# Optimization experiments

Hardware: AMD Instinct MI355X
Metric: run time of the kernel (lower is better)

## Reference

```python
import jax, jax.numpy as jnp
import numpy as np


def setup_inputs() -> dict:
    key = jax.random.key(0)
    k0, k1, k2, k3 = jax.random.split(key, 4)
    B, in_dim, n_vars, out_dim, E = 64, 512, 512, 720, 8
    x = jax.random.normal(k0, (B, in_dim, n_vars), dtype=jnp.float32)
    # Gating: nn.Linear(in_dim, E, bias=False) -> weight [E, in_dim]
    Wg = jax.random.normal(k1, (E, in_dim), dtype=jnp.float32) * 0.02
    # Experts: nn.Linear(in_dim, out_dim) -> weight [out_dim, in_dim], bias [out_dim]
    We = jax.random.normal(k2, (E, out_dim, in_dim), dtype=jnp.float32) * 0.02
    be = jax.random.normal(k3, (E, out_dim), dtype=jnp.float32) * 0.02
    return {"x": x, "Wg": Wg, "We": We, "be": be, "top_k": 2}


def reference(x, Wg, We, be, top_k):
    # x: [B, in_len, n_vars] -> tokens along n_vars with feature dim in_len
    xt = jnp.swapaxes(x, 1, 2)                      # [B, V, D]
    gate = jax.nn.softmax(xt @ Wg.T, axis=-1)       # [B, V, E]
    weights, sel = jax.lax.top_k(gate, top_k)       # [B, V, k]
    E, O, D = We.shape
    out = jnp.zeros(xt.shape[:2] + (O,), dtype=xt.dtype)  # [B, V, O]
    for e in range(E):
        # combine weight for expert e: sum over top-k slots routed to e
        coef = jnp.sum(jnp.where(sel == e, weights, jnp.zeros_like(weights)), axis=-1)  # [B, V]
        out = out + coef[..., None] * (jnp.einsum('bvd,od->bvo', xt, We[e]) + be[e])
    return jnp.swapaxes(out, 1, 2)                  # [B, pred_len, n_vars]
```

## Files before the change

### kernel.cpp

```cpp
#include <hip/hip_runtime.h>
#include <hip/hip_bf16.h>

#define DID 512
#define NV  512
#define NB  64
#define OD  720
#define OPAD 768
#define NE  8
#define NTOK (NB * NV)
#define MAXTILE 512

typedef short  bf16x8 __attribute__((ext_vector_type(8)));
typedef float  f32x4  __attribute__((ext_vector_type(4)));

#define XT_OFF    0u
#define WB_OFF    33554432u
#define PID_OFF   39845888u
#define C1D_OFF   39976960u
#define C2D_OFF   40108032u
#define TL_OFF    40239104u
#define CL1_OFF   40370176u
#define CL2_OFF   40501248u
#define BCNT_OFF  40632320u
#define BFILL_OFF 40632576u
#define BOFF_OFF  40632832u
#define TPID_OFF  40633088u
#define TT0_OFF   40635136u
#define TEND_OFF  40637184u
#define NT_OFF    40639232u
#define SCR_OFF   40639488u
#define SCR_END   87825408u

static __device__ __forceinline__ ushort f2bf(float f) {
  unsigned u = __float_as_uint(f);
  unsigned r = (u + 0x7fffu + ((u >> 16) & 1u)) >> 16;
  return (ushort)r;
}
static __device__ __forceinline__ float bf2f(ushort u) {
  return __uint_as_float(((unsigned)u) << 16);
}
static __device__ __forceinline__ void async16(const ushort* g, ushort* l) {
  __builtin_amdgcn_global_load_lds((__attribute__((address_space(1))) void*)(g),
                                   (__attribute__((address_space(3))) void*)(l),
                                   16, 0, 0);
}
static __device__ __forceinline__ int swz(int r) { return (r & 3) ^ ((r >> 2) & 1); }

__global__ __launch_bounds__(256) void k_transpose(const float* __restrict__ x,
                                                   ushort* __restrict__ xt) {
  __shared__ float s[32][33];
  const int b  = blockIdx.z;
  const int v0 = blockIdx.x * 32;
  const int d0 = blockIdx.y * 32;
  const int tx = threadIdx.x & 31;
  const int ty = threadIdx.x >> 5;
  const float* xp = x + ((size_t)b * DID + d0 + ty) * NV + v0 + tx;
#pragma unroll
  for (int i = 0; i < 4; ++i) s[ty + i * 8][tx] = xp[(size_t)i * 8 * NV];
  __syncthreads();
#pragma unroll
  for (int i = 0; i < 4; ++i) {
    int vl = ty + i * 8;
    xt[((size_t)b * NV + v0 + vl) * DID + d0 + tx] = f2bf(s[tx][vl]);
  }
}

__global__ __launch_bounds__(256) void k_wbconv(const float* __restrict__ We,
                                                ushort* __restrict__ wb) {
  const int e = blockIdx.y;
  const int i = blockIdx.x * 256 + threadIdx.x;
  const int o = i >> 9;
  ushort val = 0;
  if (o < OD) val = f2bf(We[(size_t)e * OD * DID + i]);
  wb[(size_t)e * OPAD * DID + i] = val;
}

__global__ __launch_bounds__(256) void k_gate(const float* __restrict__ x,
                                              const float* __restrict__ Wg,
                                              int* __restrict__ pairid,
                                              float* __restrict__ c1d,
                                              float* __restrict__ c2d,
                                              int* __restrict__ bcnt) {
  __shared__ float wg[NE * DID];
  __shared__ int cnt64[64];
  const int tid = threadIdx.x;
  for (int i = tid; i < NE * DID; i += 256) wg[i] = Wg[i];
  if (tid < 64) cnt64[tid] = 0;
  __syncthreads();

  const int b = blockIdx.y;
  const int v = blockIdx.x * 256 + tid;
  const float* xp = x + (size_t)b * DID * NV + v;

  float acc[NE];
#pragma unroll
  for (int e = 0; e < NE; ++e) acc[e] = 0.f;
  for (int d = 0; d < DID; d += 4) {
    float x0 = xp[(size_t)(d + 0) * NV];
    float x1 = xp[(size_t)(d + 1) * NV];
    float x2 = xp[(size_t)(d + 2) * NV];
    float x3 = xp[(size_t)(d + 3) * NV];
#pragma unroll
    for (int e = 0; e < NE; ++e) {
      float4 w4 = *(const float4*)&wg[e * DID + d];
      acc[e] += x0 * w4.x + x1 * w4.y + x2 * w4.z + x3 * w4.w;
    }
  }
  float mx = acc[0];
#pragma unroll
  for (int e = 1; e < NE; ++e) mx = fmaxf(mx, acc[e]);
  float sum = 0.f;
#pragma unroll
  for (int e = 0; e < NE; ++e) { acc[e] = __expf(acc[e] - mx); sum += acc[e]; }
  const float inv = 1.f / sum;

  int i1 = 0; float g1 = acc[0];
#pragma unroll
  for (int e = 1; e < NE; ++e) if (acc[e] > g1) { g1 = acc[e]; i1 = e; }
  int i2 = -1; float g2 = -1.f;
#pragma unroll
  for (int e = 0; e < NE; ++e) if (e != i1 && acc[e] > g2) { g2 = acc[e]; i2 = e; }
  g1 *= inv; g2 *= inv;

  int ea, eb; float ca, cb;
  if (i1 < i2) { ea = i1; eb = i2; ca = g1; cb = g2; }
  else         { ea = i2; eb = i1; ca = g2; cb = g1; }
  const int pid = ea * 8 + eb;
  const int t = b * NV + v;
  pairid[t] = pid; c1d[t] = ca; c2d[t] = cb;
  atomicAdd(&cnt64[pid], 1);
  __syncthreads();
  if (tid < 64 && cnt64[tid]) atomicAdd(&bcnt[tid], cnt64[tid]);
}

__global__ void k_prefix(const int* __restrict__ bcnt, int* __restrict__ boffs,
                         int* __restrict__ tpid, int* __restrict__ tt0,
                         int* __restrict__ tend, int* __restrict__ ntp) {
  if (threadIdx.x != 0) return;
  int off = 0, nt = 0;
  for (int p = 0; p < 64; ++p) {
    boffs[p] = off;
    const int c = bcnt[p];
    const int end = off + c;
    for (int i = 0; i * 128 < c; ++i) {
      tpid[nt] = p; tt0[nt] = off + i * 128; tend[nt] = end; ++nt;
    }
    off = end;
  }
  ntp[0] = nt;
}

__global__ __launch_bounds__(256) void k_scatter(const int* __restrict__ pairid,
                                                 const float* __restrict__ c1d,
                                                 const float* __restrict__ c2d,
                                                 const int* __restrict__ boffs,
                                                 int* __restrict__ bfill,
                                                 int* __restrict__ tlist,
                                                 float* __restrict__ cl1,
                                                 float* __restrict__ cl2) {
  __shared__ int cnt64[64], base64[64];
  const int tid = threadIdx.x;
  if (tid < 64) cnt64[tid] = 0;
  __syncthreads();
  const int t = blockIdx.x * 256 + tid;
  const int pid = pairid[t];
  const int p = atomicAdd(&cnt64[pid], 1);
  __syncthreads();
  if (tid < 64) base64[tid] = cnt64[tid] ? atomicAdd(&bfill[tid], cnt64[tid]) : 0;
  __syncthreads();
  const int slot = boffs[pid] + base64[pid] + p;
  tlist[slot] = t; cl1[slot] = c1d[t]; cl2[slot] = c2d[t];
}

__global__ __launch_bounds__(256, 2) void k_gemm(
    const ushort* __restrict__ xt, const ushort* __restrict__ wb,
    const float* __restrict__ be, const int* __restrict__ tlist,
    const float* __restrict__ cl1, const float* __restrict__ cl2,
    const int* __restrict__ tpid, const int* __restrict__ tt0,
    const int* __restrict__ tendarr, const int* __restrict__ ntp,
    ushort* __restrict__ scratch, float* __restrict__ out, int mode) {
  const int tile = blockIdx.x;
  if (tile >= ntp[0]) return;
  const int pid  = tpid[tile];
  const int t0   = tt0[tile];
  const int tend = tendarr[tile];
  const int e1 = pid >> 3, e2 = pid & 7;
  const int o0 = blockIdx.y * 128;

  __shared__ __align__(16) ushort As[2][4096];
  __shared__ __align__(16) ushort Bs[2][4096];

  const int tid  = threadIdx.x;
  const int lane = tid & 63;
  const int w    = tid >> 6;

  const int f0 = w * 128 + lane, f1 = f0 + 64;
  const int r0 = f0 >> 2, p0 = f0 & 3, q0 = p0 ^ swz(r0);
  const int r1 = f1 >> 2, p1 = f1 & 3, q1 = p1 ^ swz(r1);

  const int aoff0 = (o0 + r0) * DID + q0 * 8;
  const int aoff1 = (o0 + r1) * DID + q1 * 8;
  const int sl0 = t0 + r0, sl1 = t0 + r1;
  const int tok0 = (sl0 < tend) ? tlist[sl0] : 0;
  const int tok1 = (sl1 < tend) ? tlist[sl1] : 0;
  const int boff0 = tok0 * DID + q0 * 8;
  const int boff1 = tok1 * DID + q1 * 8;
  const int dA0 = w * 1024, dA1 = w * 1024 + 512;

  const int m    = lane & 15;
  const int quad = lane >> 4;
  const int wo   = (w >> 1) * 64;
  const int wt   = (w & 1) * 64;

  f32x4 acc[4][4];
#pragma unroll
  for (int i = 0; i < 4; ++i)
#pragma unroll
    for (int j = 0; j < 4; ++j) acc[i][j] = (f32x4){0.f, 0.f, 0.f, 0.f};

  {
    const ushort* wA = wb + (size_t)e1 * OPAD * DID;
    async16(wA + aoff0, &As[0][dA0]);
    async16(wA + aoff1, &As[0][dA1]);
    async16(xt + boff0, &Bs[0][dA0]);
    async16(xt + boff1, &Bs[0][dA1]);
  }

  for (int kk = 0; kk < 32; ++kk) {
    __syncthreads();

    if (kk == 16) {
      float ratio[4];
#pragma unroll
      for (int j = 0; j < 4; ++j) {
        const int sl = t0 + wt + j * 16 + m;
        const bool g = sl < tend;
        const float cc1 = g ? cl1[sl] : 0.f;
        const float cc2 = g ? cl2[sl] : 1.f;
        ratio[j] = cc1 / cc2;
      }
      const float* be1p = be + e1 * OD;
#pragma unroll
      for (int i = 0; i < 4; ++i) {
        const int ob = o0 + wo + i * 16 + quad * 4;
        float b0 = 0, b1 = 0, b2 = 0, b3 = 0;
        if (ob < OD) { b0 = be1p[ob]; b1 = be1p[ob + 1]; b2 = be1p[ob + 2]; b3 = be1p[ob + 3]; }
#pragma unroll
        for (int j = 0; j < 4; ++j) {
          acc[i][j][0] = (acc[i][j][0] + b0) * ratio[j];
          acc[i][j][1] = (acc[i][j][1] + b1) * ratio[j];
          acc[i][j][2] = (acc[i][j][2] + b2) * ratio[j];
          acc[i][j][3] = (acc[i][j][3] + b3) * ratio[j];
        }
      }
    }

    const int nk = kk + 1;
    if (nk < 32) {
      const int nb = nk & 1;
      const int eA = (nk < 16) ? e1 : e2;
      const int k0 = (nk & 15) * 32;
      const ushort* wA = wb + (size_t)eA * OPAD * DID + k0;
      async16(wA + aoff0, &As[nb][dA0]);
      async16(wA + aoff1, &As[nb][dA1]);
      async16(xt + boff0 + k0, &Bs[nb][dA0]);
      async16(xt + boff1 + k0, &Bs[nb][dA1]);
    }

    const int cb = kk & 1;
    bf16x8 af[4], bfr[4];
#pragma unroll
    for (int i = 0; i < 4; ++i) {
      const int R = wo + i * 16 + m;
      af[i] = *(const bf16x8*)(&As[cb][R * 32 + ((quad ^ swz(R)) << 3)]);
    }
#pragma unroll
    for (int j = 0; j < 4; ++j) {
      const int R = wt + j * 16 + m;
      bfr[j] = *(const bf16x8*)(&Bs[cb][R * 32 + ((quad ^ swz(R)) << 3)]);
    }
#pragma unroll
    for (int i = 0; i < 4; ++i)
#pragma unroll
      for (int j = 0; j < 4; ++j)
        acc[i][j] = __builtin_amdgcn_mfma_f32_16x16x32_bf16(af[i], bfr[j],
                                                            acc[i][j], 0, 0, 0);
  }

  float c2v[4]; int tokv[4]; bool gv[4];
#pragma unroll
  for (int j = 0; j < 4; ++j) {
    const int sl = t0 + wt + j * 16 + m;
    gv[j] = sl < tend;
    c2v[j]  = gv[j] ? cl2[sl] : 0.f;
    tokv[j] = gv[j] ? tlist[sl] : 0;
  }
  const float* be2p = be + e2 * OD;
#pragma unroll
  for (int i = 0; i < 4; ++i) {
    const int ob = o0 + wo + i * 16 + quad * 4;
    if (ob < OD) {
      const float b0 = be2p[ob], b1 = be2p[ob + 1], b2 = be2p[ob + 2], b3 = be2p[ob + 3];
#pragma unroll
      for (int j = 0; j < 4; ++j) {
        if (gv[j]) {
          const float v0 = c2v[j] * (acc[i][j][0] + b0);
          const float v1 = c2v[j] * (acc[i][j][1] + b1);
          const float v2 = c2v[j] * (acc[i][j][2] + b2);
          const float v3 = c2v[j] * (acc[i][j][3] + b3);
          if (mode == 0) {
            ushort4 pk = make_ushort4(f2bf(v0), f2bf(v1), f2bf(v2), f2bf(v3));
            *(ushort4*)(scratch + (size_t)tokv[j] * OD + ob) = pk;
          } else {
            const int bb = tokv[j] >> 9, vv = tokv[j] & 511;
            float* op = out + ((size_t)bb * OD + ob) * NV + vv;
            op[0] = v0; op[(size_t)NV] = v1; op[2 * (size_t)NV] = v2; op[3 * (size_t)NV] = v3;
          }
        }
      }
    }
  }
}

__global__ __launch_bounds__(256) void k_combine(const ushort* __restrict__ scratch,
                                                 float* __restrict__ out) {
  __shared__ ushort s[64][68];
  const int v0 = blockIdx.x * 64;
  const int o0 = blockIdx.y * 64;
  const int b  = blockIdx.z;
  const int tid = threadIdx.x;
#pragma unroll
  for (int it = 0; it < 2; ++it) {
    const int c = it * 256 + tid;
    const int row = c >> 3, cg = c & 7;
    const int o = o0 + cg * 8;
    if (o + 8 <= OD) {
      const ushort* src = scratch + ((size_t)(b * NV + v0 + row)) * OD + o;
      ushort4 ua = *(const ushort4*)(src);
      ushort4 ub = *(const ushort4*)(src + 4);
      *(ushort4*)&s[row][cg * 8] = ua;
      *(ushort4*)&s[row][cg * 8 + 4] = ub;
    }
  }
  __syncthreads();
  const int vv = tid & 63;
  const int og = tid >> 6;
#pragma unroll
  for (int oi = 0; oi < 8; ++oi) {
    const int ol = (og * 8 + oi) * 2;
    const int o = o0 + ol;
    if (o < OD) {
      ushort2 u = *(const ushort2*)&s[vv][ol];
      float* op = out + ((size_t)b * OD + o) * NV + v0 + vv;
      op[0]  = bf2f(u.x);
      op[NV] = bf2f(u.y);
    }
  }
}

extern "C" void kernel_launch(void* const* d_in, const int* in_sizes, int n_in,
                              void* d_out, int out_size, void* d_ws, size_t ws_size,
                              hipStream_t stream) {
  const float* x  = (const float*)d_in[0];
  const float* Wg = (const float*)d_in[1];
  const float* We = (const float*)d_in[2];
  const float* be = (const float*)d_in[3];
  float* out = (float*)d_out;

  char* ws = (char*)d_ws;
  ushort* xt     = (ushort*)(ws + XT_OFF);
  ushort* wb     = (ushort*)(ws + WB_OFF);
  int*    pairid = (int*)   (ws + PID_OFF);
  float*  c1d    = (float*) (ws + C1D_OFF);
  float*  c2d    = (float*) (ws + C2D_OFF);
  int*    tlist  = (int*)   (ws + TL_OFF);
  float*  cl1    = (float*) (ws + CL1_OFF);
  float*  cl2    = (float*) (ws + CL2_OFF);
  int*    bcnt   = (int*)   (ws + BCNT_OFF);
  int*    bfill  = (int*)   (ws + BFILL_OFF);
  int*    boffs  = (int*)   (ws + BOFF_OFF);
  int*    tpid   = (int*)   (ws + TPID_OFF);
  int*    tt0    = (int*)   (ws + TT0_OFF);
  int*    tend   = (int*)   (ws + TEND_OFF);
  int*    ntp    = (int*)   (ws + NT_OFF);
  ushort* scratch= (ushort*)(ws + SCR_OFF);

  const int mode = (ws_size >= (size_t)SCR_END) ? 0 : 1;

  (void)hipMemsetAsync(bcnt, 0, 512, stream);

  k_transpose<<<dim3(NV / 32, DID / 32, NB), 256, 0, stream>>>(x, xt);
  k_wbconv<<<dim3(OPAD * DID / 256, NE), 256, 0, stream>>>(We, wb);
  k_gate<<<dim3(NV / 256, NB), 256, 0, stream>>>(x, Wg, pairid, c1d, c2d, bcnt);
  k_prefix<<<1, 64, 0, stream>>>(bcnt, boffs, tpid, tt0, tend, ntp);
  k_scatter<<<NTOK / 256, 256, 0, stream>>>(pairid, c1d, c2d, boffs, bfill,
                                            tlist, cl1, cl2);
  k_gemm<<<dim3(320, OPAD / 128), 256, 0, stream>>>(xt, wb, be, tlist, cl1, cl2,
                                                    tpid, tt0, tend, ntp,
                                                    scratch, out, mode);
  if (mode == 0)
    k_combine<<<dim3(NV / 64, (OD + 63) / 64, NB), 256, 0, stream>>>(scratch, out);
}
```

Before: 340.2 us.

## Fuse prep kernels, parallelize prefix scan, reorder GEMM grid, unswizzled LDS layout

Merges the transpose, weight conversion and counter memset into one k_prep launch. It also replaces the serial single-thread prefix with a wave-level shuffle scan, and swaps the GEMM grid axes so consecutive blocks share a token tile across output tiles. The GEMM LDS staging now uses a fragment-ordered layout, so each lane reads its MFMA operand contiguously with no XOR swizzle. Together these cut launch count and serial latency and improve L2 reuse of gathered activations. In exchange, the counter zeroing now relies on k_prep fully completing before k_gate runs.

```diff
diff --git a/kernel.cpp b/kernel.cpp
--- a/kernel.cpp
+++ b/kernel.cpp
@@ -44,35 +44,41 @@
                                    (__attribute__((address_space(3))) void*)(l),
                                    16, 0, 0);
 }
-static __device__ __forceinline__ int swz(int r) { return (r & 3) ^ ((r >> 2) & 1); }
-
-__global__ __launch_bounds__(256) void k_transpose(const float* __restrict__ x,
-                                                   ushort* __restrict__ xt) {
-  __shared__ float s[32][33];
-  const int b  = blockIdx.z;
-  const int v0 = blockIdx.x * 32;
-  const int d0 = blockIdx.y * 32;
-  const int tx = threadIdx.x & 31;
-  const int ty = threadIdx.x >> 5;
-  const float* xp = x + ((size_t)b * DID + d0 + ty) * NV + v0 + tx;
-#pragma unroll
-  for (int i = 0; i < 4; ++i) s[ty + i * 8][tx] = xp[(size_t)i * 8 * NV];
-  __syncthreads();
-#pragma unroll
-  for (int i = 0; i < 4; ++i) {
-    int vl = ty + i * 8;
-    xt[((size_t)b * NV + v0 + vl) * DID + d0 + tx] = f2bf(s[tx][vl]);
-  }
-}
-
-__global__ __launch_bounds__(256) void k_wbconv(const float* __restrict__ We,
-                                                ushort* __restrict__ wb) {
-  const int e = blockIdx.y;
-  const int i = blockIdx.x * 256 + threadIdx.x;
-  const int o = i >> 9;
-  ushort val = 0;
-  if (o < OD) val = f2bf(We[(size_t)e * OD * DID + i]);
-  wb[(size_t)e * OPAD * DID + i] = val;
+
+__global__ __launch_bounds__(256) void k_prep(const float* __restrict__ x,
+                                              ushort* __restrict__ xt,
+                                              const float* __restrict__ We,
+                                              ushort* __restrict__ wb,
+                                              int* __restrict__ bcnt) {
+  const int tid = threadIdx.x;
+  if (blockIdx.z < 64) {
+    if (blockIdx.z == 0 && blockIdx.x == 0 && blockIdx.y == 0 && tid < 128)
+      bcnt[tid] = 0;
+    __shared__ float s[32][33];
+    const int b  = blockIdx.z;
+    const int v0 = blockIdx.x * 32;
+    const int d0 = blockIdx.y * 32;
+    const int tx = tid & 31;
+    const int ty = tid >> 5;
+    const float* xp = x + ((size_t)b * DID + d0 + ty) * NV + v0 + tx;
+#pragma unroll
+    for (int i = 0; i < 4; ++i) s[ty + i * 8][tx] = xp[(size_t)i * 8 * NV];
+    __syncthreads();
+#pragma unroll
+    for (int i = 0; i < 4; ++i) {
+      int vl = ty + i * 8;
+      xt[((size_t)b * NV + v0 + vl) * DID + d0 + tx] = f2bf(s[tx][vl]);
+    }
+  } else {
+    const int e = blockIdx.z - 64;
+    int i = (blockIdx.y * 16 + blockIdx.x) * 256 + tid;
+    for (; i < OPAD * DID; i += 65536) {
+      const int o = i >> 9;
+      ushort val = 0;
+      if (o < OD) val = f2bf(We[(size_t)e * OD * DID + i]);
+      wb[(size_t)e * OPAD * DID + i] = val;
+    }
+  }
 }
 
 __global__ __launch_bounds__(256) void k_gate(const float* __restrict__ x,
@@ -136,18 +142,28 @@
 __global__ void k_prefix(const int* __restrict__ bcnt, int* __restrict__ boffs,
                          int* __restrict__ tpid, int* __restrict__ tt0,
                          int* __restrict__ tend, int* __restrict__ ntp) {
-  if (threadIdx.x != 0) return;
-  int off = 0, nt = 0;
-  for (int p = 0; p < 64; ++p) {
-    boffs[p] = off;
-    const int c = bcnt[p];
-    const int end = off + c;
-    for (int i = 0; i * 128 < c; ++i) {
-      tpid[nt] = p; tt0[nt] = off + i * 128; tend[nt] = end; ++nt;
-    }
-    off = end;
-  }
-  ntp[0] = nt;
+  const int p = threadIdx.x;
+  const int c = bcnt[p];
+  int inc = c;
+#pragma unroll
+  for (int d = 1; d < 64; d <<= 1) {
+    int n = __shfl_up(inc, d, 64);
+    if (p >= d) inc += n;
+  }
+  const int off = inc - c;
+  boffs[p] = off;
+  const int tc = (c + 127) >> 7;
+  int inct = tc;
+#pragma unroll
+  for (int d = 1; d < 64; d <<= 1) {
+    int n = __shfl_up(inct, d, 64);
+    if (p >= d) inct += n;
+  }
+  const int tb = inct - tc;
+  for (int i = 0; i < tc; ++i) {
+    tpid[tb + i] = p; tt0[tb + i] = off + i * 128; tend[tb + i] = off + c;
+  }
+  if (p == 63) ntp[0] = inct;
 }
 
 __global__ __launch_bounds__(256) void k_scatter(const int* __restrict__ pairid,
@@ -179,13 +195,13 @@
     const int* __restrict__ tpid, const int* __restrict__ tt0,
     const int* __restrict__ tendarr, const int* __restrict__ ntp,
     ushort* __restrict__ scratch, float* __restrict__ out, int mode) {
-  const int tile = blockIdx.x;
+  const int tile = blockIdx.y;
   if (tile >= ntp[0]) return;
   const int pid  = tpid[tile];
   const int t0   = tt0[tile];
   const int tend = tendarr[tile];
   const int e1 = pid >> 3, e2 = pid & 7;
-  const int o0 = blockIdx.y * 128;
+  const int o0 = blockIdx.x * 128;
 
   __shared__ __align__(16) ushort As[2][4096];
   __shared__ __align__(16) ushort Bs[2][4096];
@@ -193,24 +209,28 @@
   const int tid  = threadIdx.x;
   const int lane = tid & 63;
   const int w    = tid >> 6;
-
-  const int f0 = w * 128 + lane, f1 = f0 + 64;
-  const int r0 = f0 >> 2, p0 = f0 & 3, q0 = p0 ^ swz(r0);
-  const int r1 = f1 >> 2, p1 = f1 & 3, q1 = p1 ^ swz(r1);
-
-  const int aoff0 = (o0 + r0) * DID + q0 * 8;
-  const int aoff1 = (o0 + r1) * DID + q1 * 8;
-  const int sl0 = t0 + r0, sl1 = t0 + r1;
-  const int tok0 = (sl0 < tend) ? tlist[sl0] : 0;
-  const int tok1 = (sl1 < tend) ? tlist[sl1] : 0;
-  const int boff0 = tok0 * DID + q0 * 8;
-  const int boff1 = tok1 * DID + q1 * 8;
-  const int dA0 = w * 1024, dA1 = w * 1024 + 512;
+  const int m16  = lane & 15;
+  const int ch   = lane >> 4;
+
+  const int rA0 = 2 * w * 16 + m16;
+  const int sl0 = t0 + rA0, sl1 = sl0 + 16;
+  const int tk0 = (sl0 < tend) ? tlist[sl0] : 0;
+  const int tk1 = (sl1 < tend) ? tlist[sl1] : 0;
+
+  const size_t eStride = (size_t)OPAD * DID;
+  const int    aoff    = (o0 + rA0) * DID + ch * 8;
+  const ushort* gb0 = xt + (size_t)tk0 * DID + ch * 8;
+  const ushort* gb1 = xt + (size_t)tk1 * DID + ch * 8;
+
+  const int dst0 = 2 * w * 512 + lane * 8;
+  const int dst1 = dst0 + 512;
 
   const int m    = lane & 15;
   const int quad = lane >> 4;
   const int wo   = (w >> 1) * 64;
   const int wt   = (w & 1) * 64;
+  const int fa   = (w >> 1) * 4;
+  const int fb   = (w & 1) * 4;
 
   f32x4 acc[4][4];
 #pragma unroll
@@ -219,11 +239,11 @@
     for (int j = 0; j < 4; ++j) acc[i][j] = (f32x4){0.f, 0.f, 0.f, 0.f};
 
   {
-    const ushort* wA = wb + (size_t)e1 * OPAD * DID;
-    async16(wA + aoff0, &As[0][dA0]);
-    async16(wA + aoff1, &As[0][dA1]);
-    async16(xt + boff0, &Bs[0][dA0]);
-    async16(xt + boff1, &Bs[0][dA1]);
+    const ushort* wA = wb + (size_t)e1 * eStride + aoff;
+    async16(wA, &As[0][dst0]);
+    async16(wA + 16 * DID, &As[0][dst1]);
+    async16(gb0, &Bs[0][dst0]);
+    async16(gb1, &Bs[0][dst1]);
   }
 
   for (int kk = 0; kk < 32; ++kk) {
@@ -260,25 +280,21 @@
       const int nb = nk & 1;
       const int eA = (nk < 16) ? e1 : e2;
       const int k0 = (nk & 15) * 32;
-      const ushort* wA = wb + (size_t)eA * OPAD * DID + k0;
-      async16(wA + aoff0, &As[nb][dA0]);
-      async16(wA + aoff1, &As[nb][dA1]);
-      async16(xt + boff0 + k0, &Bs[nb][dA0]);
-      async16(xt + boff1 + k0, &Bs[nb][dA1]);
+      const ushort* wA = wb + (size_t)eA * eStride + aoff + k0;
+      async16(wA, &As[nb][dst0]);
+      async16(wA + 16 * DID, &As[nb][dst1]);
+      async16(gb0 + k0, &Bs[nb][dst0]);
+      async16(gb1 + k0, &Bs[nb][dst1]);
     }
 
     const int cb = kk & 1;
     bf16x8 af[4], bfr[4];
 #pragma unroll
-    for (int i = 0; i < 4; ++i) {
-      const int R = wo + i * 16 + m;
-      af[i] = *(const bf16x8*)(&As[cb][R * 32 + ((quad ^ swz(R)) << 3)]);
-    }
-#pragma unroll
-    for (int j = 0; j < 4; ++j) {
-      const int R = wt + j * 16 + m;
-      bfr[j] = *(const bf16x8*)(&Bs[cb][R * 32 + ((quad ^ swz(R)) << 3)]);
-    }
+    for (int i = 0; i < 4; ++i)
+      af[i] = *(const bf16x8*)(&As[cb][(fa + i) * 512 + lane * 8]);
+#pragma unroll
+    for (int j = 0; j < 4; ++j)
+      bfr[j] = *(const bf16x8*)(&Bs[cb][(fb + j) * 512 + lane * 8]);
 #pragma unroll
     for (int i = 0; i < 4; ++i)
 #pragma unroll
@@ -387,15 +403,12 @@
 
   const int mode = (ws_size >= (size_t)SCR_END) ? 0 : 1;
 
-  (void)hipMemsetAsync(bcnt, 0, 512, stream);
-
-  k_transpose<<<dim3(NV / 32, DID / 32, NB), 256, 0, stream>>>(x, xt);
-  k_wbconv<<<dim3(OPAD * DID / 256, NE), 256, 0, stream>>>(We, wb);
+  k_prep<<<dim3(16, 16, 72), 256, 0, stream>>>(x, xt, We, wb, bcnt);
   k_gate<<<dim3(NV / 256, NB), 256, 0, stream>>>(x, Wg, pairid, c1d, c2d, bcnt);
   k_prefix<<<1, 64, 0, stream>>>(bcnt, boffs, tpid, tt0, tend, ntp);
   k_scatter<<<NTOK / 256, 256, 0, stream>>>(pairid, c1d, c2d, boffs, bfill,
                                             tlist, cl1, cl2);
-  k_gemm<<<dim3(320, OPAD / 128), 256, 0, stream>>>(xt, wb, be, tlist, cl1, cl2,
+  k_gemm<<<dim3(OPAD / 128, 320), 256, 0, stream>>>(xt, wb, be, tlist, cl1, cl2,
                                                     tpid, tt0, tend, ntp,
                                                     scratch, out, mode);
   if (mode == 0)
```

Result: slower. 359.2 us (+5.6%).
